# Performance work log

Hardware: AMD Instinct MI355X
Metric: run time of the kernel (lower is better)

The kernel has to match this reference:

```python
import jax, jax.numpy as jnp
import numpy as np

B, N, C = 8, 1024, 768
H = 12
DH = C // H  # 64
FF = 3072
EPS = 1e-5


def _layer_norm(x, gamma, beta):
    mu = jnp.mean(x, axis=-1, keepdims=True)
    var = jnp.mean(jnp.square(x - mu), axis=-1, keepdims=True)
    return (x - mu) * jax.lax.rsqrt(var + EPS) * gamma + beta


def setup_inputs() -> dict:
    key = jax.random.key(0)
    ks = jax.random.split(key, 16)
    s_in = 1.0 / np.sqrt(C)
    s_ff = 1.0 / np.sqrt(FF)
    return {
        "x": jax.random.normal(ks[0], (B, N, C), dtype=jnp.float32),
        "Wq": jax.random.uniform(ks[1], (C, C), jnp.float32, -s_in, s_in),
        "bq": jax.random.uniform(ks[2], (C,), jnp.float32, -s_in, s_in),
        "Wk": jax.random.uniform(ks[3], (C, C), jnp.float32, -s_in, s_in),
        "bk": jax.random.uniform(ks[4], (C,), jnp.float32, -s_in, s_in),
        "Wv": jax.random.uniform(ks[5], (C, C), jnp.float32, -s_in, s_in),
        "bv": jax.random.uniform(ks[6], (C,), jnp.float32, -s_in, s_in),
        "Wo": jax.random.uniform(ks[7], (C, C), jnp.float32, -s_in, s_in),
        "bo": jax.random.uniform(ks[8], (C,), jnp.float32, -s_in, s_in),
        "g1": jnp.ones((C,), jnp.float32),
        "b1": jnp.zeros((C,), jnp.float32),
        "g2": jnp.ones((C,), jnp.float32),
        "b2": jnp.zeros((C,), jnp.float32),
        "W1": jax.random.uniform(ks[9], (C, FF), jnp.float32, -s_in, s_in),
        "bf1": jax.random.uniform(ks[10], (FF,), jnp.float32, -s_in, s_in),
        "W2": jax.random.uniform(ks[11], (FF, C), jnp.float32, -s_ff, s_ff),
        "bf2": jax.random.uniform(ks[12], (C,), jnp.float32, -s_ff, s_ff),
    }


def reference(x, Wq, bq, Wk, bk, Wv, bv, Wo, bo, g1, b1, g2, b2, W1, bf1, W2, bf2):
    # Pre-norm attention block
    xn = _layer_norm(x, g1, b1)
    q = (xn @ Wq + bq).reshape(B, N, H, DH)
    k = (xn @ Wk + bk).reshape(B, N, H, DH)
    v = (xn @ Wv + bv).reshape(B, N, H, DH)
    scores = jnp.einsum("bqhd,bkhd->bhqk", q, k) / np.sqrt(DH)  # [B,H,N,N]
    attn = jax.nn.softmax(scores, axis=-1)
    z = jnp.einsum("bhqk,bkhd->bqhd", attn, v).reshape(B, N, C)
    attn_out = z @ Wo + bo
    b = x + attn_out  # dropout is identity (p=0 / eval)
    # Pre-norm MLP block
    bn = _layer_norm(b, g2, b2)
    h = jax.nn.relu(bn @ W1 + bf1)
    y = b + (h @ W2 + bf2)
    return y
```

## Files before the change

kernel.cpp:

```cpp
#include <hip/hip_runtime.h>
#include <hip/hip_bf16.h>

#define BDIM 8
#define SEQ  1024
#define CH   768
#define NHD  12
#define DHD  64
#define FFD  3072
#define MR   (BDIM*SEQ)

typedef __attribute__((ext_vector_type(8))) short bf16x8;
typedef __attribute__((ext_vector_type(4))) float f32x4;
typedef unsigned int   u32;
typedef unsigned short u16;

__device__ __forceinline__ u16 f2bfu(float x) {
  __hip_bfloat16 h = __float2bfloat16(x);
  return *reinterpret_cast<u16*>(&h);
}

__device__ __forceinline__ void glds16(const void* g, void* l) {
  __builtin_amdgcn_global_load_lds(
      (const __attribute__((address_space(1))) u32*)g,
      (__attribute__((address_space(3))) u32*)l, 16, 0, 0);
}

__global__ __launch_bounds__(256) void k_transpose_all(
    const float* __restrict__ Wq, const float* __restrict__ Wk,
    const float* __restrict__ Wv, const float* __restrict__ Wo,
    const float* __restrict__ W1, const float* __restrict__ W2,
    u16* __restrict__ ws) {
  __shared__ float tile[32][33];
  int b = blockIdx.x;
  int id, tb;
  if (b < 2304)      { id = b / 576; tb = b % 576; }
  else if (b < 4608) { id = 4;       tb = b - 2304; }
  else               { id = 5;       tb = b - 4608; }
  const float* src;
  u16* dst;
  int K, Nc;
  switch (id) {
    case 0: src = Wq; dst = ws;                      K = CH;  Nc = CH;  break;
    case 1: src = Wk; dst = ws + (size_t)CH*CH;      K = CH;  Nc = CH;  break;
    case 2: src = Wv; dst = ws + (size_t)2*CH*CH;    K = CH;  Nc = CH;  break;
    case 3: src = Wo; dst = ws + (size_t)3*CH*CH;    K = CH;  Nc = CH;  break;
    case 4: src = W1; dst = ws + (size_t)4*CH*CH;    K = CH;  Nc = FFD; break;
    default:src = W2; dst = ws + (size_t)4*CH*CH + (size_t)CH*FFD;
                                                     K = FFD; Nc = CH;  break;
  }
  int tilesx = Nc >> 5;
  int bx = (tb % tilesx) * 32;
  int by = (tb / tilesx) * 32;
  int tx = threadIdx.x & 31, ty = threadIdx.x >> 5;
#pragma unroll
  for (int j = 0; j < 32; j += 8)
    tile[ty + j][tx] = src[(size_t)(by + ty + j) * Nc + bx + tx];
  __syncthreads();
#pragma unroll
  for (int j = 0; j < 32; j += 8)
    dst[(size_t)(bx + ty + j) * K + by + tx] = f2bfu(tile[tx][ty + j]);
}

__global__ __launch_bounds__(256) void k_pack_bias(
    const float* __restrict__ bq, const float* __restrict__ bk,
    const float* __restrict__ bv, float* __restrict__ dst) {
  int i = blockIdx.x * 256 + threadIdx.x;
  if (i < 3 * CH)
    dst[i] = i < CH ? bq[i] : (i < 2 * CH ? bk[i - CH] : bv[i - 2 * CH]);
}

__global__ __launch_bounds__(256) void k_layernorm_bf16(
    const float* __restrict__ src, const float* __restrict__ gamma,
    const float* __restrict__ beta, u16* __restrict__ dst) {
  int row  = blockIdx.x * 4 + (threadIdx.x >> 6);
  int lane = threadIdx.x & 63;
  const float4* p4 = (const float4*)(src + (size_t)row * CH);
  float4 v[3];
  float s = 0.f, s2 = 0.f;
#pragma unroll
  for (int k = 0; k < 3; k++) {
    v[k] = p4[lane + k * 64];
    s  += v[k].x + v[k].y + v[k].z + v[k].w;
    s2 += v[k].x * v[k].x + v[k].y * v[k].y + v[k].z * v[k].z + v[k].w * v[k].w;
  }
#pragma unroll
  for (int m = 1; m < 64; m <<= 1) {
    s  += __shfl_xor(s,  m, 64);
    s2 += __shfl_xor(s2, m, 64);
  }
  float mean = s * (1.f / CH);
  float var  = s2 * (1.f / CH) - mean * mean;
  float rs   = rsqrtf(var + 1e-5f);
  u16* drow = dst + (size_t)row * CH;
#pragma unroll
  for (int k = 0; k < 3; k++) {
    int col = lane * 4 + k * 256;
    float4 gq = ((const float4*)gamma)[lane + k * 64];
    float4 bq = ((const float4*)beta )[lane + k * 64];
    u32 lo = (u32)f2bfu((v[k].x - mean) * rs * gq.x + bq.x) |
             ((u32)f2bfu((v[k].y - mean) * rs * gq.y + bq.y) << 16);
    u32 hi = (u32)f2bfu((v[k].z - mean) * rs * gq.z + bq.z) |
             ((u32)f2bfu((v[k].w - mean) * rs * gq.w + bq.w) << 16);
    uint2 w; w.x = lo; w.y = hi;
    *(uint2*)(drow + col) = w;
  }
}

enum { EPI_QKV = 0, EPI_RESID = 1, EPI_RELU = 2 };

template <int EPI>
__device__ __forceinline__ void gemm_epi(const f32x4& a, int row0, int col,
                                         float bval, const float* resid,
                                         void* outp, int Nmat) {
  if constexpr (EPI == EPI_QKV) {
    int sel = col / CH;
    int c = col - sel * CH;
    int h = c >> 6, d = c & 63;
    int bb = row0 >> 10, nn0 = row0 & (SEQ - 1);
    if (sel == 2) {
      union { uint2 u; u16 h4[4]; } pk;
#pragma unroll
      for (int r = 0; r < 4; r++) pk.h4[r] = f2bfu(a[r] + bval);
      *(uint2*)&((u16*)outp)[(size_t)2 * MR * CH +
                             (((size_t)(bb * NHD + h)) * DHD + d) * SEQ + nn0] =
          pk.u;
    } else {
#pragma unroll
      for (int r = 0; r < 4; r++)
        ((u16*)outp)[(size_t)sel * MR * CH +
                     (((size_t)(bb * NHD + h)) * SEQ + nn0 + r) * DHD + d] =
            f2bfu(a[r] + bval);
    }
  } else if constexpr (EPI == EPI_RESID) {
#pragma unroll
    for (int r = 0; r < 4; r++) {
      size_t idx = (size_t)(row0 + r) * Nmat + col;
      ((float*)outp)[idx] = a[r] + bval + resid[idx];
    }
  } else {
#pragma unroll
    for (int r = 0; r < 4; r++) {
      float val = a[r] + bval;
      ((u16*)outp)[(size_t)(row0 + r) * Nmat + col] =
          f2bfu(val > 0.f ? val : 0.f);
    }
  }
}

template <int EPI, int TM = 128>
__global__ __launch_bounds__(256, 2) void k_gemm(
    const u16* __restrict__ A, const u16* __restrict__ Bt,
    const float* __restrict__ bias, const float* __restrict__ resid,
    void* __restrict__ outp, int K, int Nmat) {
  __shared__ u16 As[2][TM * 32];
  __shared__ u16 Bs[2][128 * 32];
  constexpr int MF = TM / 32;
  int tid = threadIdx.x;
  int bm = blockIdx.x, bn = blockIdx.y;
  int lane = tid & 63, wid = tid >> 6;
  int wr = (wid >> 1) * (TM / 2), wc = (wid & 1) * 64;
  int lrow = lane & 15, g = lane >> 4;

  const u16* Abase = A + (size_t)(bm * TM) * K;
  const u16* Bbase = Bt + (size_t)(bn * 128) * K;

  auto stage = [&](int buf, int k0) {
#pragma unroll
    for (int r = 0; r < TM / 64; r++) {
      int c = tid + r * 256;
      int row = c >> 2;
      int scol = ((c & 3) ^ ((row >> 1) & 3)) * 8;
      glds16(Abase + (size_t)row * K + k0 + scol, &As[buf][c * 8]);
    }
#pragma unroll
    for (int r = 0; r < 2; r++) {
      int c = tid + r * 256;
      int row = c >> 2;
      int scol = ((c & 3) ^ ((row >> 1) & 3)) * 8;
      glds16(Bbase + (size_t)row * K + k0 + scol, &Bs[buf][c * 8]);
    }
  };

  int xsl = (g ^ ((lrow >> 1) & 3)) * 8;

  f32x4 acc[MF][4];
#pragma unroll
  for (int m = 0; m < MF; m++)
#pragma unroll
    for (int n = 0; n < 4; n++) acc[m][n] = {0.f, 0.f, 0.f, 0.f};

  int nk = K >> 5;
  stage(0, 0);
  for (int kt = 0; kt < nk; ++kt) {
    int buf = kt & 1;
    __syncthreads();
    if (kt + 1 < nk) stage(buf ^ 1, (kt + 1) << 5);
    bf16x8 af[MF], bfr[4];
#pragma unroll
    for (int m = 0; m < MF; m++)
      af[m] = *(const bf16x8*)&As[buf][(wr + m * 16 + lrow) * 32 + xsl];
#pragma unroll
    for (int n = 0; n < 4; n++)
      bfr[n] = *(const bf16x8*)&Bs[buf][(wc + n * 16 + lrow) * 32 + xsl];
    __builtin_amdgcn_s_setprio(1);
#pragma unroll
    for (int m = 0; m < MF; m++)
#pragma unroll
      for (int n = 0; n < 4; n++)
        acc[m][n] = __builtin_amdgcn_mfma_f32_16x16x32_bf16(af[m], bfr[n],
                                                            acc[m][n], 0, 0, 0);
    __builtin_amdgcn_s_setprio(0);
  }

#pragma unroll
  for (int m = 0; m < MF; m++) {
    int row0 = bm * TM + wr + m * 16 + g * 4;
#pragma unroll
    for (int n = 0; n < 4; n++) {
      int col = bn * 128 + wc + n * 16 + lrow;
      gemm_epi<EPI>(acc[m][n], row0, col, bias[col], resid, outp, Nmat);
    }
  }
}

__global__ __launch_bounds__(512, 4) void k_attn(
    const u16* __restrict__ Q, const u16* __restrict__ Kk,
    const u16* __restrict__ Vt, u16* __restrict__ Z) {
  __shared__ u16 Ks[2][64 * 64];
  __shared__ u16 Vs[2][64 * 64];
  __shared__ u32 Psu[8][64 * 9];
  int tid = threadIdx.x, lane = tid & 63, wid = tid >> 6;
  int lrow = lane & 15, g = lane >> 4;
  int id  = blockIdx.x;
  int nid = (id & 7) * 96 + (id >> 3);
  int bh = nid >> 3;
  int qtile = (nid & 7) * 128;
  size_t base = (size_t)bh * SEQ * DHD;
  int bb = bh / NHD, hh = bh % NHD;
  int qrow0 = qtile + wid * 16;

  bf16x8 qf[2];
#pragma unroll
  for (int ks = 0; ks < 2; ks++)
    qf[ks] = *(const bf16x8*)(Q + base + (size_t)(qrow0 + lrow) * DHD +
                              ks * 32 + g * 8);

  f32x4 accO[4];
  float mrun = -1e30f, lrun = 0.f;
#pragma unroll
  for (int n = 0; n < 4; n++) accO[n] = {0.f, 0.f, 0.f, 0.f};

  int srow = tid >> 3;
  int swz  = (((tid & 7) * 16) ^ ((srow & 7) << 4)) >> 1;
  const u16* kg0 = Kk + base + (size_t)srow * DHD + swz;
  const u16* vg0 = Vt + base + (size_t)srow * SEQ + swz;

  auto stageKV = [&](int buf, int t) {
    glds16(kg0 + (size_t)t * 64 * DHD, &Ks[buf][tid * 8]);
    glds16(vg0 + t * 64,               &Vs[buf][tid * 8]);
  };

  int rc0 = ((g * 16)      ^ ((lrow & 7) << 4)) >> 1;
  int rc1 = ((64 + g * 16) ^ ((lrow & 7) << 4)) >> 1;

  stageKV(0, 0);
  for (int t = 0; t < 16; ++t) {
    int buf = t & 1;
    __syncthreads();
    if (t + 1 < 16) stageKV(buf ^ 1, t + 1);

    f32x4 sacc[4];
    __builtin_amdgcn_s_setprio(1);
#pragma unroll
    for (int n = 0; n < 4; n++) {
      bf16x8 kf0 = *(const bf16x8*)&Ks[buf][(n * 16 + lrow) * 64 + rc0];
      bf16x8 kf1 = *(const bf16x8*)&Ks[buf][(n * 16 + lrow) * 64 + rc1];
      sacc[n] = {0.f, 0.f, 0.f, 0.f};
      sacc[n] = __builtin_amdgcn_mfma_f32_16x16x32_bf16(kf0, qf[0], sacc[n], 0, 0, 0);
      sacc[n] = __builtin_amdgcn_mfma_f32_16x16x32_bf16(kf1, qf[1], sacc[n], 0, 0, 0);
    }
    __builtin_amdgcn_s_setprio(0);

    float mx = fmaxf(fmaxf(fmaxf(sacc[0][0], sacc[0][1]),
                           fmaxf(sacc[0][2], sacc[0][3])),
                     fmaxf(fmaxf(sacc[1][0], sacc[1][1]),
                           fmaxf(sacc[1][2], sacc[1][3])));
    mx = fmaxf(mx, fmaxf(fmaxf(fmaxf(sacc[2][0], sacc[2][1]),
                               fmaxf(sacc[2][2], sacc[2][3])),
                         fmaxf(fmaxf(sacc[3][0], sacc[3][1]),
                               fmaxf(sacc[3][2], sacc[3][3]))));
    mx *= 0.125f;
    mx = fmaxf(mx, __shfl_xor(mx, 16, 64));
    mx = fmaxf(mx, __shfl_xor(mx, 32, 64));

    if (__all(mx <= mrun + 8.f)) {
      float psum = 0.f;
#pragma unroll
      for (int n = 0; n < 4; n++)
#pragma unroll
        for (int r = 0; r < 4; r++) {
          float p = __expf(sacc[n][r] * 0.125f - mrun);
          sacc[n][r] = p;
          psum += p;
        }
      psum += __shfl_xor(psum, 16, 64);
      psum += __shfl_xor(psum, 32, 64);
      lrun += psum;
    } else {
      float mnew = fmaxf(mrun, mx);
      float alpha = __expf(mrun - mnew);
      float psum = 0.f;
#pragma unroll
      for (int n = 0; n < 4; n++)
#pragma unroll
        for (int r = 0; r < 4; r++) {
          float p = __expf(sacc[n][r] * 0.125f - mnew);
          sacc[n][r] = p;
          psum += p;
        }
      psum += __shfl_xor(psum, 16, 64);
      psum += __shfl_xor(psum, 32, 64);
      lrun = lrun * alpha + psum;
      mrun = mnew;
#pragma unroll
      for (int r = 0; r < 4; r++) {
        float ar = __shfl(alpha, (lane & 48) | (g * 4 + r), 64);
#pragma unroll
        for (int n = 0; n < 4; n++) accO[n][r] *= ar;
      }
    }

#pragma unroll
    for (int n = 0; n < 4; n++) {
      u32 lo = (u32)f2bfu(sacc[n][0]) | ((u32)f2bfu(sacc[n][1]) << 16);
      u32 hi = (u32)f2bfu(sacc[n][2]) | ((u32)f2bfu(sacc[n][3]) << 16);
      Psu[wid][lane * 9 + 2 * n]     = lo;
      Psu[wid][lane * 9 + 2 * n + 1] = hi;
    }

    int laneA = lrow + ((g & 1) << 5);
    int laneB = laneA + 16;
    int nsel = g >> 1;
    __builtin_amdgcn_s_setprio(1);
#pragma unroll
    for (int ks = 0; ks < 2; ks++) {
      int nks = 2 * ks + nsel;
      union { bf16x8 v; u32 w[4]; } pk;
      pk.w[0] = Psu[wid][laneA * 9 + 2 * nks];
      pk.w[1] = Psu[wid][laneA * 9 + 2 * nks + 1];
      pk.w[2] = Psu[wid][laneB * 9 + 2 * nks];
      pk.w[3] = Psu[wid][laneB * 9 + 2 * nks + 1];
      int rc = ks ? rc1 : rc0;
#pragma unroll
      for (int n = 0; n < 4; n++) {
        bf16x8 vf = *(const bf16x8*)&Vs[buf][(n * 16 + lrow) * 64 + rc];
        accO[n] = __builtin_amdgcn_mfma_f32_16x16x32_bf16(pk.v, vf,
                                                          accO[n], 0, 0, 0);
      }
    }
    __builtin_amdgcn_s_setprio(0);
  }

#pragma unroll
  for (int r = 0; r < 4; r++) {
    float lr = __shfl(lrun, (lane & 48) | (g * 4 + r), 64);
    float inv = 1.f / lr;
    int qrow = qrow0 + g * 4 + r;
#pragma unroll
    for (int n = 0; n < 4; n++) {
      int d = n * 16 + lrow;
      Z[((size_t)(bb * SEQ + qrow)) * CH + hh * DHD + d] =
          f2bfu(accO[n][r] * inv);
    }
  }
}

extern "C" void kernel_launch(void* const* d_in, const int* in_sizes, int n_in,
                              void* d_out, int out_size, void* d_ws,
                              size_t ws_size, hipStream_t stream) {
  (void)in_sizes; (void)n_in; (void)out_size; (void)ws_size;
  const float* x   = (const float*)d_in[0];
  const float* Wq  = (const float*)d_in[1];
  const float* bq  = (const float*)d_in[2];
  const float* Wk  = (const float*)d_in[3];
  const float* bk  = (const float*)d_in[4];
  const float* Wv  = (const float*)d_in[5];
  const float* bv  = (const float*)d_in[6];
  const float* Wo  = (const float*)d_in[7];
  const float* bo  = (const float*)d_in[8];
  const float* g1  = (const float*)d_in[9];
  const float* b1  = (const float*)d_in[10];
  const float* g2  = (const float*)d_in[11];
  const float* b2  = (const float*)d_in[12];
  const float* W1  = (const float*)d_in[13];
  const float* bf1 = (const float*)d_in[14];
  const float* W2  = (const float*)d_in[15];
  const float* bf2 = (const float*)d_in[16];

  u16* wsu  = (u16*)d_ws;
  u16* wq_t = wsu;
  u16* wo_t = wq_t + (size_t)3 * CH * CH;
  u16* w1_t = wo_t + (size_t)CH * CH;
  u16* w2_t = w1_t + (size_t)CH * FFD;
  u16* xn   = w2_t + (size_t)CH * FFD;
  u16* qb   = xn + (size_t)MR * CH;
  u16* zb   = qb + (size_t)3 * MR * CH;
  float* bres = (float*)(zb + (size_t)MR * CH);
  u16* hb   = qb;
  float* bqkv = (float*)d_out;

  dim3 blk(256);
  k_transpose_all<<<6912, blk, 0, stream>>>(Wq, Wk, Wv, Wo, W1, W2, wsu);
  k_pack_bias<<<9, blk, 0, stream>>>(bq, bk, bv, bqkv);

  k_layernorm_bf16<<<2048, blk, 0, stream>>>(x, g1, b1, xn);
  k_gemm<EPI_QKV, 128><<<dim3(64, 18), blk, 0, stream>>>(
      xn, wq_t, bqkv, nullptr, qb, CH, 3 * CH);
  k_attn<<<768, dim3(512), 0, stream>>>(qb, qb + (size_t)MR * CH,
                                        qb + (size_t)2 * MR * CH, zb);
  k_gemm<EPI_RESID, 64><<<dim3(128, 6), blk, 0, stream>>>(
      zb, wo_t, bo, x, bres, CH, CH);
  k_layernorm_bf16<<<2048, blk, 0, stream>>>(bres, g2, b2, xn);
  k_gemm<EPI_RELU, 128><<<dim3(64, 24), blk, 0, stream>>>(
      xn, w1_t, bf1, nullptr, hb, CH, FFD);
  k_gemm<EPI_RESID, 64><<<dim3(128, 6), blk, 0, stream>>>(
      hb, w2_t, bf2, bres, (float*)d_out, FFD, CH);
}
```

Measured before the change: 262.1 us.

## Add triple-buffered 128x128 GEMM kernel for MLP projections

Adds a new GEMM kernel with a three-stage LDS ring buffer using direct global-to-LDS loads, a K-tile of 32, and a single barrier per iteration, and uses it for both MLP GEMMs. The second MLP GEMM moves from 64-row to 128-row tiles, halving its grid to 384 blocks. The goal is to hide global-load latency behind MFMA work and to reuse each tile more. The cost is more LDS per block, lower occupancy, and fewer blocks for the down projection, which may underfill the GPU.

```diff
diff --git a/kernel.cpp b/kernel.cpp
--- a/kernel.cpp
+++ b/kernel.cpp
@@ -223,6 +223,87 @@
   }
 }
 
+template <int EPI>
+__global__ __launch_bounds__(256, 3) void k_gemmr(
+    const u16* __restrict__ A, const u16* __restrict__ Bt,
+    const float* __restrict__ bias, const float* __restrict__ resid,
+    void* __restrict__ outp, int K, int Nmat) {
+  __shared__ u16 As[3][128 * 32];
+  __shared__ u16 Bs[3][128 * 32];
+  int tid = threadIdx.x;
+  int bm = blockIdx.x, bn = blockIdx.y;
+  int lane = tid & 63, wid = tid >> 6;
+  int wr = (wid >> 1) * 64, wc = (wid & 1) * 64;
+  int lrow = lane & 15, g = lane >> 4;
+
+  const u16* Abase = A + (size_t)(bm * 128) * K;
+  const u16* Bbase = Bt + (size_t)(bn * 128) * K;
+
+  auto stage = [&](int slot, int kt) {
+    int k0 = kt << 5;
+#pragma unroll
+    for (int r = 0; r < 2; r++) {
+      int c = tid + r * 256;
+      int row = c >> 2;
+      int scol = ((c & 3) ^ ((row >> 1) & 3)) * 8;
+      glds16(Abase + (size_t)row * K + k0 + scol, &As[slot][c * 8]);
+    }
+#pragma unroll
+    for (int r = 0; r < 2; r++) {
+      int c = tid + r * 256;
+      int row = c >> 2;
+      int scol = ((c & 3) ^ ((row >> 1) & 3)) * 8;
+      glds16(Bbase + (size_t)row * K + k0 + scol, &Bs[slot][c * 8]);
+    }
+  };
+
+  int xsl = (g ^ ((lrow >> 1) & 3)) * 8;
+
+  f32x4 acc[4][4];
+#pragma unroll
+  for (int m = 0; m < 4; m++)
+#pragma unroll
+    for (int n = 0; n < 4; n++) acc[m][n] = {0.f, 0.f, 0.f, 0.f};
+
+  int NK = K >> 5;
+  stage(0, 0);
+  stage(1, 1);
+  for (int t = 0; t < NK; ++t) {
+    int slot = t % 3;
+    if (t < NK - 1) asm volatile("s_waitcnt vmcnt(4)" ::: "memory");
+    else            asm volatile("s_waitcnt vmcnt(0)" ::: "memory");
+    __builtin_amdgcn_s_barrier();
+    __builtin_amdgcn_sched_barrier(0);
+    if (t + 2 < NK) stage((t + 2) % 3, t + 2);
+
+    bf16x8 af[4], bfv[4];
+#pragma unroll
+    for (int mf = 0; mf < 4; mf++)
+      af[mf] = *(const bf16x8*)&As[slot][(wr + mf * 16 + lrow) * 32 + xsl];
+#pragma unroll
+    for (int nf = 0; nf < 4; nf++)
+      bfv[nf] = *(const bf16x8*)&Bs[slot][(wc + nf * 16 + lrow) * 32 + xsl];
+    __builtin_amdgcn_s_setprio(1);
+#pragma unroll
+    for (int mf = 0; mf < 4; mf++)
+#pragma unroll
+      for (int nf = 0; nf < 4; nf++)
+        acc[mf][nf] = __builtin_amdgcn_mfma_f32_16x16x32_bf16(
+            af[mf], bfv[nf], acc[mf][nf], 0, 0, 0);
+    __builtin_amdgcn_s_setprio(0);
+  }
+
+#pragma unroll
+  for (int mf = 0; mf < 4; mf++) {
+    int row0 = bm * 128 + wr + mf * 16 + g * 4;
+#pragma unroll
+    for (int nf = 0; nf < 4; nf++) {
+      int col = bn * 128 + wc + nf * 16 + lrow;
+      gemm_epi<EPI>(acc[mf][nf], row0, col, bias[col], resid, outp, Nmat);
+    }
+  }
+}
+
 __global__ __launch_bounds__(512, 4) void k_attn(
     const u16* __restrict__ Q, const u16* __restrict__ Kk,
     const u16* __restrict__ Vt, u16* __restrict__ Z) {
@@ -421,8 +502,8 @@
   k_gemm<EPI_RESID, 64><<<dim3(128, 6), blk, 0, stream>>>(
       zb, wo_t, bo, x, bres, CH, CH);
   k_layernorm_bf16<<<2048, blk, 0, stream>>>(bres, g2, b2, xn);
-  k_gemm<EPI_RELU, 128><<<dim3(64, 24), blk, 0, stream>>>(
+  k_gemmr<EPI_RELU><<<dim3(64, 24), blk, 0, stream>>>(
       xn, w1_t, bf1, nullptr, hb, CH, FFD);
-  k_gemm<EPI_RESID, 64><<<dim3(128, 6), blk, 0, stream>>>(
+  k_gemmr<EPI_RESID><<<dim3(64, 6), blk, 0, stream>>>(
       hb, w2_t, bf2, bres, (float*)d_out, FFD, CH);
 }
```

Result: slower. 267.6 us (+2.1%).

## Replace GEMM with 512-thread 128x256 tile, triple-buffered BK=64 pipeline

Applied to the files above, without the earlier changes.

Replaces the 256-thread double-buffered GEMM with an 8-wave kernel using 128x256 output tiles, K-step 64, and a three-stage LDS ring. The next-next stage is prefetched in two halves between half-K MFMA phases, with explicit vmcnt waits and raw barriers. The aim is to hide global-load latency and raise MFMA density per LDS byte. In exchange, LDS use is much larger (about 144 KB per block), and the grids for the N=768 GEMMs shrink to 192 blocks, which may underfill the 256 CUs.

```diff
diff --git a/kernel.cpp b/kernel.cpp
--- a/kernel.cpp
+++ b/kernel.cpp
@@ -147,78 +147,114 @@
   }
 }
 
-template <int EPI, int TM = 128>
-__global__ __launch_bounds__(256, 2) void k_gemm(
+template <int EPI>
+__global__ __launch_bounds__(512, 2) void k_gemm8(
     const u16* __restrict__ A, const u16* __restrict__ Bt,
     const float* __restrict__ bias, const float* __restrict__ resid,
     void* __restrict__ outp, int K, int Nmat) {
-  __shared__ u16 As[2][TM * 32];
-  __shared__ u16 Bs[2][128 * 32];
-  constexpr int MF = TM / 32;
+  __shared__ u16 AL[3][128 * 64];
+  __shared__ u16 BL[3][256 * 64];
   int tid = threadIdx.x;
   int bm = blockIdx.x, bn = blockIdx.y;
   int lane = tid & 63, wid = tid >> 6;
-  int wr = (wid >> 1) * (TM / 2), wc = (wid & 1) * 64;
+  int wm = wid >> 2, wn = wid & 3;
   int lrow = lane & 15, g = lane >> 4;
 
-  const u16* Abase = A + (size_t)(bm * TM) * K;
-  const u16* Bbase = Bt + (size_t)(bn * 128) * K;
-
-  auto stage = [&](int buf, int k0) {
-#pragma unroll
-    for (int r = 0; r < TM / 64; r++) {
-      int c = tid + r * 256;
-      int row = c >> 2;
-      int scol = ((c & 3) ^ ((row >> 1) & 3)) * 8;
-      glds16(Abase + (size_t)row * K + k0 + scol, &As[buf][c * 8]);
-    }
-#pragma unroll
-    for (int r = 0; r < 2; r++) {
-      int c = tid + r * 256;
-      int row = c >> 2;
-      int scol = ((c & 3) ^ ((row >> 1) & 3)) * 8;
-      glds16(Bbase + (size_t)row * K + k0 + scol, &Bs[buf][c * 8]);
-    }
+  const u16* Abase = A + (size_t)(bm * 128) * K;
+  const u16* Bbase = Bt + (size_t)(bn * 256) * K;
+
+  auto stA = [&](int s, int kt, int r) {
+    int u = tid + r * 512;
+    int row = u >> 3, slot = u & 7;
+    glds16(Abase + (size_t)row * K + (kt << 6) + (((slot ^ (row & 7))) << 3),
+           &AL[s][u * 8]);
   };
-
-  int xsl = (g ^ ((lrow >> 1) & 3)) * 8;
-
-  f32x4 acc[MF][4];
-#pragma unroll
-  for (int m = 0; m < MF; m++)
+  auto stB = [&](int s, int kt, int r) {
+    int u = tid + r * 512;
+    int row = u >> 3, slot = u & 7;
+    glds16(Bbase + (size_t)row * K + (kt << 6) + (((slot ^ (row & 7))) << 3),
+           &BL[s][u * 8]);
+  };
+
+  int arow = wm * 64 + lrow;
+  int brow = wn * 64 + lrow;
+  int swz = lrow & 7;
+  int x0 = ((g) ^ swz) * 8;
+  int x1 = ((4 + g) ^ swz) * 8;
+
+  f32x4 acc[4][4];
+#pragma unroll
+  for (int m = 0; m < 4; m++)
 #pragma unroll
     for (int n = 0; n < 4; n++) acc[m][n] = {0.f, 0.f, 0.f, 0.f};
 
-  int nk = K >> 5;
-  stage(0, 0);
-  for (int kt = 0; kt < nk; ++kt) {
-    int buf = kt & 1;
-    __syncthreads();
-    if (kt + 1 < nk) stage(buf ^ 1, (kt + 1) << 5);
-    bf16x8 af[MF], bfr[4];
-#pragma unroll
-    for (int m = 0; m < MF; m++)
-      af[m] = *(const bf16x8*)&As[buf][(wr + m * 16 + lrow) * 32 + xsl];
-#pragma unroll
-    for (int n = 0; n < 4; n++)
-      bfr[n] = *(const bf16x8*)&Bs[buf][(wc + n * 16 + lrow) * 32 + xsl];
-    __builtin_amdgcn_s_setprio(1);
-#pragma unroll
-    for (int m = 0; m < MF; m++)
+  int NK = K >> 6;
+#pragma unroll
+  for (int r = 0; r < 2; r++) stA(0, 0, r);
+#pragma unroll
+  for (int r = 0; r < 4; r++) stB(0, 0, r);
+#pragma unroll
+  for (int r = 0; r < 2; r++) stA(1, 1, r);
+#pragma unroll
+  for (int r = 0; r < 4; r++) stB(1, 1, r);
+
+  for (int kt = 0; kt < NK; ++kt) {
+    int s = kt % 3, sn = (kt + 2) % 3;
+    bool pre = (kt + 2) < NK;
+    if (kt < NK - 1) asm volatile("s_waitcnt vmcnt(6)" ::: "memory");
+    else             asm volatile("s_waitcnt vmcnt(0)" ::: "memory");
+    __builtin_amdgcn_s_barrier();
+    __builtin_amdgcn_sched_barrier(0);
+
+    if (pre) { stA(sn, kt + 2, 0); stA(sn, kt + 2, 1);
+               stB(sn, kt + 2, 0); stB(sn, kt + 2, 1); }
+    {
+      bf16x8 af[4], bf[4];
+#pragma unroll
+      for (int mi = 0; mi < 4; mi++)
+        af[mi] = *(const bf16x8*)&AL[s][(arow + mi * 16) * 64 + x0];
 #pragma unroll
       for (int n = 0; n < 4; n++)
-        acc[m][n] = __builtin_amdgcn_mfma_f32_16x16x32_bf16(af[m], bfr[n],
-                                                            acc[m][n], 0, 0, 0);
-    __builtin_amdgcn_s_setprio(0);
-  }
-
-#pragma unroll
-  for (int m = 0; m < MF; m++) {
-    int row0 = bm * TM + wr + m * 16 + g * 4;
+        bf[n] = *(const bf16x8*)&BL[s][(brow + n * 16) * 64 + x0];
+      __builtin_amdgcn_s_setprio(1);
+#pragma unroll
+      for (int mi = 0; mi < 4; mi++)
+#pragma unroll
+        for (int n = 0; n < 4; n++)
+          acc[mi][n] = __builtin_amdgcn_mfma_f32_16x16x32_bf16(
+              af[mi], bf[n], acc[mi][n], 0, 0, 0);
+      __builtin_amdgcn_s_setprio(0);
+    }
+    __builtin_amdgcn_s_barrier();
+    __builtin_amdgcn_sched_barrier(0);
+
+    if (pre) { stB(sn, kt + 2, 2); stB(sn, kt + 2, 3); }
+    {
+      bf16x8 af[4], bf[4];
+#pragma unroll
+      for (int mi = 0; mi < 4; mi++)
+        af[mi] = *(const bf16x8*)&AL[s][(arow + mi * 16) * 64 + x1];
+#pragma unroll
+      for (int n = 0; n < 4; n++)
+        bf[n] = *(const bf16x8*)&BL[s][(brow + n * 16) * 64 + x1];
+      __builtin_amdgcn_s_setprio(1);
+#pragma unroll
+      for (int mi = 0; mi < 4; mi++)
+#pragma unroll
+        for (int n = 0; n < 4; n++)
+          acc[mi][n] = __builtin_amdgcn_mfma_f32_16x16x32_bf16(
+              af[mi], bf[n], acc[mi][n], 0, 0, 0);
+      __builtin_amdgcn_s_setprio(0);
+    }
+  }
+
+#pragma unroll
+  for (int mi = 0; mi < 4; mi++) {
+    int row0 = bm * 128 + wm * 64 + mi * 16 + g * 4;
 #pragma unroll
     for (int n = 0; n < 4; n++) {
-      int col = bn * 128 + wc + n * 16 + lrow;
-      gemm_epi<EPI>(acc[m][n], row0, col, bias[col], resid, outp, Nmat);
+      int col = bn * 256 + wn * 64 + n * 16 + lrow;
+      gemm_epi<EPI>(acc[mi][n], row0, col, bias[col], resid, outp, Nmat);
     }
   }
 }
@@ -414,15 +450,15 @@
   k_pack_bias<<<9, blk, 0, stream>>>(bq, bk, bv, bqkv);
 
   k_layernorm_bf16<<<2048, blk, 0, stream>>>(x, g1, b1, xn);
-  k_gemm<EPI_QKV, 128><<<dim3(64, 18), blk, 0, stream>>>(
+  k_gemm8<EPI_QKV><<<dim3(64, 9), dim3(512), 0, stream>>>(
       xn, wq_t, bqkv, nullptr, qb, CH, 3 * CH);
   k_attn<<<768, dim3(512), 0, stream>>>(qb, qb + (size_t)MR * CH,
                                         qb + (size_t)2 * MR * CH, zb);
-  k_gemm<EPI_RESID, 64><<<dim3(128, 6), blk, 0, stream>>>(
+  k_gemm8<EPI_RESID><<<dim3(64, 3), dim3(512), 0, stream>>>(
       zb, wo_t, bo, x, bres, CH, CH);
   k_layernorm_bf16<<<2048, blk, 0, stream>>>(bres, g2, b2, xn);
-  k_gemm<EPI_RELU, 128><<<dim3(64, 24), blk, 0, stream>>>(
+  k_gemm8<EPI_RELU><<<dim3(64, 12), dim3(512), 0, stream>>>(
       xn, w1_t, bf1, nullptr, hb, CH, FFD);
-  k_gemm<EPI_RESID, 64><<<dim3(128, 6), blk, 0, stream>>>(
+  k_gemm8<EPI_RESID><<<dim3(64, 3), dim3(512), 0, stream>>>(
       hb, w2_t, bf2, bres, (float*)d_out, FFD, CH);
 }
```

New measurement: 318.2 us. 1.21x slower.
